# Kernel optimization log

Hardware: AMD Instinct MI355X
Metric: run time of the kernel (lower is better)

## Reference

```python
import jax, jax.numpy as jnp
import numpy as np

B, F, NL = 4096, 1024, 24          # batch, layer width (=in/out features), num hidden layers
TOTAL = F * (NL + 2)               # total DAG nodes: sources + NL hidden ranks + sinks(=last rank)


def setup_inputs() -> dict:
    key = jax.random.key(0)
    k1, k2, k3 = jax.random.split(key, 3)
    x = jax.random.normal(k1, (B, F), jnp.float32)
    # weights incl. bias row; kaiming-ish scale
    W = jax.random.normal(k2, (NL, F + 1, F), jnp.float32) * (1.0 / np.sqrt(F))
    # random 0/1 connectivity mask (requires_grad=False in original); bias row always 1
    M = jax.random.bernoulli(k3, 0.5, (NL, F + 1, F)).astype(jnp.float32)
    M = M.at[:, -1, :].set(1.0)
    sources = jnp.arange(F, dtype=jnp.int32)
    rank = jnp.arange(NL, dtype=jnp.int32)[:, None]
    col = jnp.arange(F, dtype=jnp.int32)[None, :]
    layers_idx = (rank + 1) * F + col   # node ids of rank i+1
    preds_idx = rank * F + col          # predecessors = previous rank
    return {"x": x, "W": W, "M": M, "sources": sources,
            "layers_idx": layers_idx, "preds_idx": preds_idx}


def reference(x, W, M, sources, layers_idx, preds_idx):
    # activations buffer over all DAG nodes
    acts = jnp.zeros((x.shape[0], TOTAL), x.dtype)
    acts = acts.at[:, sources].set(x)
    ones = jnp.ones((x.shape[0], 1), x.dtype)  # bias column

    def step(acts, layer):
        Wi, Mi, li, pi = layer
        h = jnp.concatenate([acts[:, pi], ones], axis=1)   # gather preds + bias
        out = jax.nn.relu(h @ (Mi * Wi))                    # masked GEMM + activation
        acts = acts.at[:, li].set(out)                      # scatter into node activations
        return acts, None

    acts, _ = jax.lax.scan(step, acts, (W, M, layers_idx, preds_idx))
    return acts[:, layers_idx[-1]]  # sinks = last rank
```

## Files before the change

kernel.cpp:

```cpp
#include <hip/hip_runtime.h>
#include <cstdint>
#include <cstddef>

#define NLAYERS 24
#define BATCH   4096
#define FEAT    1024

typedef _Float16 half_t;
typedef half_t half8 __attribute__((ext_vector_type(8)));
typedef float  f32x4 __attribute__((ext_vector_type(4)));

__device__ __forceinline__ void gload_lds16(const void* g, void* l) {
    __builtin_amdgcn_global_load_lds(
        (__attribute__((address_space(1))) void*)(void*)g,
        (__attribute__((address_space(3))) void*)l,
        16, 0, 0);
}

__global__ __launch_bounds__(256) void prep_weights(
    const float* __restrict__ W, const float* __restrict__ M,
    half_t* __restrict__ WmT)
{
    __shared__ float tile[64][65];

    const int bid = blockIdx.x;
    const int l   = bid >> 8;
    const int t   = bid & 255;
    const int k0  = (t >> 4) * 64;
    const int n0  = (t & 15) * 64;
    const size_t lbase = (size_t)l * 1025 * 1024;

    const int tid = threadIdx.x;
    const int rr  = tid >> 4;
    const int c4  = (tid & 15) * 4;

#pragma unroll
    for (int i = 0; i < 4; ++i) {
        const int row = rr + i * 16;
        const size_t g = lbase + (size_t)(k0 + row) * 1024 + (n0 + c4);
        const float4 w4 = *(const float4*)(W + g);
        const float4 m4 = *(const float4*)(M + g);
        tile[row][c4 + 0] = w4.x * m4.x;
        tile[row][c4 + 1] = w4.y * m4.y;
        tile[row][c4 + 2] = w4.z * m4.z;
        tile[row][c4 + 3] = w4.w * m4.w;
    }
    __syncthreads();

    const int n   = tid >> 2;
    const int k16 = (tid & 3) * 16;
    half8 lo, hi;
#pragma unroll
    for (int j = 0; j < 8; ++j) {
        lo[j] = (half_t)tile[k16 + j][n];
        hi[j] = (half_t)tile[k16 + 8 + j][n];
    }
    const size_t o = (size_t)l * 1024 * 1024 + (size_t)(n0 + n) * 1024 + (k0 + k16);
    *(half8*)(WmT + o)     = lo;
    *(half8*)(WmT + o + 8) = hi;
}

__global__ __launch_bounds__(256) void prep_bias(
    const float* __restrict__ W, float* __restrict__ bias)
{
    const int i = blockIdx.x * 256 + threadIdx.x;
    const int l = i >> 10;
    const int n = i & 1023;
    bias[i] = W[(size_t)l * 1025 * 1024 + (size_t)1024 * 1024 + n];
}

__global__ __launch_bounds__(256) void prep_xcast(
    const float* __restrict__ x, half_t* __restrict__ a0)
{
    const size_t i = ((size_t)blockIdx.x * 256 + threadIdx.x) * 8;
    const float4 u = *(const float4*)(x + i);
    const float4 v = *(const float4*)(x + i + 4);
    half8 h;
    h[0] = (half_t)u.x; h[1] = (half_t)u.y; h[2] = (half_t)u.z; h[3] = (half_t)u.w;
    h[4] = (half_t)v.x; h[5] = (half_t)v.y; h[6] = (half_t)v.z; h[7] = (half_t)v.w;
    *(half8*)(a0 + i) = h;
}

template <int LAST>
__global__ __launch_bounds__(256, 2) void gemm_layer(
    const half_t* __restrict__ A,
    const half_t* __restrict__ Bt,
    const float*  __restrict__ bias,
    half_t* __restrict__ Ch,
    float*  __restrict__ Cf)
{
    __shared__ half_t As[128 * 32];
    __shared__ half_t Bs[64 * 32];

    const int tid  = threadIdx.x;
    const int bid  = blockIdx.x;
    const int bm   = bid >> 4;
    const int bn   = bid & 15;
    const int lane = tid & 63;
    const int q    = lane >> 4;
    const int r    = lane & 15;
    const int w    = tid >> 6;
    const int wr   = w >> 1;
    const int wc   = w & 1;

    const half_t* Ab = A  + (size_t)bm * 128 * 1024;
    const half_t* Bb = Bt + (size_t)bn * 64 * 1024;

    const int srow = tid >> 2;
    const int scol = (tid & 3) * 8;
    const int wbase = (tid & 192) * 8;

    const int aoff = (wr * 64 + r) * 32 + q * 8;
    const int boff = (wc * 32 + r) * 32 + q * 8;

    f32x4 acc[4][2];
#pragma unroll
    for (int m = 0; m < 4; ++m)
#pragma unroll
        for (int n = 0; n < 2; ++n)
            acc[m][n] = (f32x4){0.f, 0.f, 0.f, 0.f};

    for (int kt = 0; kt < 32; ++kt) {
        const int k0 = kt * 32;
        __syncthreads();
        gload_lds16(Ab + (size_t)srow * 1024 + k0 + scol,        As + wbase);
        gload_lds16(Ab + (size_t)(64 + srow) * 1024 + k0 + scol, As + 2048 + wbase);
        gload_lds16(Bb + (size_t)srow * 1024 + k0 + scol,        Bs + wbase);
        __syncthreads();

        half8 a[4], b[2];
#pragma unroll
        for (int m = 0; m < 4; ++m) a[m] = *(const half8*)(As + aoff + m * 512);
#pragma unroll
        for (int n = 0; n < 2; ++n) b[n] = *(const half8*)(Bs + boff + n * 512);
#pragma unroll
        for (int m = 0; m < 4; ++m)
#pragma unroll
            for (int n = 0; n < 2; ++n)
                acc[m][n] = __builtin_amdgcn_mfma_f32_16x16x32_f16(a[m], b[n], acc[m][n], 0, 0, 0);
    }

    const int colb = bn * 64 + wc * 32 + r;
    const int rowb = bm * 128 + wr * 64 + q * 4;
#pragma unroll
    for (int n = 0; n < 2; ++n) {
        const int col = colb + n * 16;
        const float bv = bias[col];
#pragma unroll
        for (int m = 0; m < 4; ++m) {
            const int row = rowb + m * 16;
#pragma unroll
            for (int t = 0; t < 4; ++t) {
                float v = acc[m][n][t] + bv;
                v = v > 0.f ? v : 0.f;
                if (LAST) Cf[(size_t)(row + t) * 1024 + col] = v;
                else      Ch[(size_t)(row + t) * 1024 + col] = (half_t)v;
            }
        }
    }
}

extern "C" void kernel_launch(void* const* d_in, const int* in_sizes, int n_in,
                              void* d_out, int out_size, void* d_ws, size_t ws_size,
                              hipStream_t stream)
{
    const float* x = (const float*)d_in[0];
    const float* W = (const float*)d_in[1];
    const float* M = (const float*)d_in[2];
    float* out = (float*)d_out;

    half_t* WmT  = (half_t*)d_ws;
    float*  bias = (float*)(WmT + (size_t)NLAYERS * 1024 * 1024);
    half_t* act0 = (half_t*)(bias + NLAYERS * 1024);
    half_t* act1 = act0 + (size_t)BATCH * FEAT;

    prep_weights<<<dim3(NLAYERS * 256), dim3(256), 0, stream>>>(W, M, WmT);
    prep_bias   <<<dim3(96),            dim3(256), 0, stream>>>(W, bias);
    prep_xcast  <<<dim3(2048),          dim3(256), 0, stream>>>(x, act0);

    half_t* cur = act0;
    half_t* nxt = act1;
    for (int l = 0; l < NLAYERS; ++l) {
        const half_t* Wl = WmT + (size_t)l * 1024 * 1024;
        const float*  bl = bias + l * 1024;
        if (l == NLAYERS - 1) {
            gemm_layer<1><<<dim3(512), dim3(256), 0, stream>>>(cur, Wl, bl, (half_t*)nullptr, out);
        } else {
            gemm_layer<0><<<dim3(512), dim3(256), 0, stream>>>(cur, Wl, bl, nxt, (float*)nullptr);
        }
        half_t* tmp = cur; cur = nxt; nxt = tmp;
    }
}
```

Measured before the change: 736.2 us.

## Enlarge GEMM tile to 128x128 with double-buffered LDS and K=64 steps

The per-layer GEMM block tile grows from 128x64 to 128x128, so each wave computes 4x4 MFMA tiles and both operands get more reuse per byte loaded. LDS is now double-buffered: the next K=64 slab is staged with global_load_lds while the current one is consumed, leaving one barrier per iteration. The shared-memory layout becomes a fragment-ordered swizzle so each lane reads contiguous 16-byte chunks. In exchange, only 256 blocks are launched on a 256-CU part, and more registers and LDS per block lower occupancy.

```diff
diff --git a/kernel.cpp b/kernel.cpp
--- a/kernel.cpp
+++ b/kernel.cpp
@@ -82,20 +82,20 @@
 }
 
 template <int LAST>
-__global__ __launch_bounds__(256, 2) void gemm_layer(
+__global__ __launch_bounds__(256) void gemm_layer(
     const half_t* __restrict__ A,
     const half_t* __restrict__ Bt,
     const float*  __restrict__ bias,
     half_t* __restrict__ Ch,
     float*  __restrict__ Cf)
 {
-    __shared__ half_t As[128 * 32];
-    __shared__ half_t Bs[64 * 32];
+    __shared__ half_t As[2][8192];
+    __shared__ half_t Bs[2][8192];
 
     const int tid  = threadIdx.x;
     const int bid  = blockIdx.x;
-    const int bm   = bid >> 4;
-    const int bn   = bid & 15;
+    const int bm   = bid >> 3;
+    const int bn   = bid & 7;
     const int lane = tid & 63;
     const int q    = lane >> 4;
     const int r    = lane & 15;
@@ -104,46 +104,82 @@
     const int wc   = w & 1;
 
     const half_t* Ab = A  + (size_t)bm * 128 * 1024;
-    const half_t* Bb = Bt + (size_t)bn * 64 * 1024;
-
-    const int srow = tid >> 2;
-    const int scol = (tid & 3) * 8;
-    const int wbase = (tid & 192) * 8;
-
-    const int aoff = (wr * 64 + r) * 32 + q * 8;
-    const int boff = (wc * 32 + r) * 32 + q * 8;
-
-    f32x4 acc[4][2];
+    const half_t* Bb = Bt + (size_t)bn * 128 * 1024;
+
+    const int sc_r  = tid & 15;
+    const int sc_q8 = ((tid >> 4) & 3) * 8;
+
+    f32x4 acc[4][4];
 #pragma unroll
     for (int m = 0; m < 4; ++m)
 #pragma unroll
-        for (int n = 0; n < 2; ++n)
+        for (int n = 0; n < 4; ++n)
             acc[m][n] = (f32x4){0.f, 0.f, 0.f, 0.f};
 
-    for (int kt = 0; kt < 32; ++kt) {
-        const int k0 = kt * 32;
+#define STAGE(ABUF, BBUF, K0)                                                   \
+    {                                                                           \
+        _Pragma("unroll")                                                       \
+        for (int rd = 0; rd < 4; ++rd) {                                        \
+            const int chunk = rd * 256 + tid;                                   \
+            const int kb    = (chunk >> 6) & 1;                                 \
+            const int rb    = chunk >> 7;                                       \
+            const int row   = rb * 16 + sc_r;                                   \
+            const int kc    = (K0) + kb * 32 + sc_q8;                           \
+            const int base  = (rd * 256 + (tid & 192)) * 8;                     \
+            gload_lds16(Ab + (size_t)row * 1024 + kc, (ABUF) + base);           \
+            gload_lds16(Bb + (size_t)row * 1024 + kc, (BBUF) + base);           \
+        }                                                                       \
+    }
+
+    STAGE(As[0], Bs[0], 0)
+
+    const int lane8 = lane * 8;
+    int cur = 0;
+
+    for (int kt = 0; kt < 16; ++kt) {
         __syncthreads();
-        gload_lds16(Ab + (size_t)srow * 1024 + k0 + scol,        As + wbase);
-        gload_lds16(Ab + (size_t)(64 + srow) * 1024 + k0 + scol, As + 2048 + wbase);
-        gload_lds16(Bb + (size_t)srow * 1024 + k0 + scol,        Bs + wbase);
-        __syncthreads();
-
-        half8 a[4], b[2];
-#pragma unroll
-        for (int m = 0; m < 4; ++m) a[m] = *(const half8*)(As + aoff + m * 512);
-#pragma unroll
-        for (int n = 0; n < 2; ++n) b[n] = *(const half8*)(Bs + boff + n * 512);
+        if (kt < 15) {
+            half_t* An = As[cur ^ 1];
+            half_t* Bn = Bs[cur ^ 1];
+            const int k0n = (kt + 1) * 64;
+            STAGE(An, Bn, k0n)
+        }
+
+        const half_t* Ac = As[cur];
+        const half_t* Bc = Bs[cur];
+
+        half8 a0[4], a1[4], b0[4], b1[4];
+#pragma unroll
+        for (int m = 0; m < 4; ++m) {
+            const int sb = (wr * 4 + m) * 2;
+            a0[m] = *(const half8*)(Ac + (sb + 0) * 512 + lane8);
+            a1[m] = *(const half8*)(Ac + (sb + 1) * 512 + lane8);
+        }
+#pragma unroll
+        for (int n = 0; n < 4; ++n) {
+            const int sb = (wc * 4 + n) * 2;
+            b0[n] = *(const half8*)(Bc + (sb + 0) * 512 + lane8);
+            b1[n] = *(const half8*)(Bc + (sb + 1) * 512 + lane8);
+        }
 #pragma unroll
         for (int m = 0; m < 4; ++m)
 #pragma unroll
-            for (int n = 0; n < 2; ++n)
-                acc[m][n] = __builtin_amdgcn_mfma_f32_16x16x32_f16(a[m], b[n], acc[m][n], 0, 0, 0);
-    }
-
-    const int colb = bn * 64 + wc * 32 + r;
+            for (int n = 0; n < 4; ++n)
+                acc[m][n] = __builtin_amdgcn_mfma_f32_16x16x32_f16(a0[m], b0[n], acc[m][n], 0, 0, 0);
+#pragma unroll
+        for (int m = 0; m < 4; ++m)
+#pragma unroll
+            for (int n = 0; n < 4; ++n)
+                acc[m][n] = __builtin_amdgcn_mfma_f32_16x16x32_f16(a1[m], b1[n], acc[m][n], 0, 0, 0);
+
+        cur ^= 1;
+    }
+#undef STAGE
+
+    const int colb = bn * 128 + wc * 64 + r;
     const int rowb = bm * 128 + wr * 64 + q * 4;
 #pragma unroll
-    for (int n = 0; n < 2; ++n) {
+    for (int n = 0; n < 4; ++n) {
         const int col = colb + n * 16;
         const float bv = bias[col];
 #pragma unroll
@@ -184,9 +220,9 @@
         const half_t* Wl = WmT + (size_t)l * 1024 * 1024;
         const float*  bl = bias + l * 1024;
         if (l == NLAYERS - 1) {
-            gemm_layer<1><<<dim3(512), dim3(256), 0, stream>>>(cur, Wl, bl, (half_t*)nullptr, out);
+            gemm_layer<1><<<dim3(256), dim3(256), 0, stream>>>(cur, Wl, bl, (half_t*)nullptr, out);
         } else {
-            gemm_layer<0><<<dim3(512), dim3(256), 0, stream>>>(cur, Wl, bl, nxt, (float*)nullptr);
+            gemm_layer<0><<<dim3(256), dim3(256), 0, stream>>>(cur, Wl, bl, nxt, (float*)nullptr);
         }
         half_t* tmp = cur; cur = nxt; nxt = tmp;
     }
```

Result: slower. 1.010 ms (+37.2%).

## Double-buffer LDS tiles with K=64 stages and fragment-ordered layout

Applied to the files above, without the earlier changes.

The GEMM layer kernel now keeps two LDS buffers, so the global-to-LDS loads for the next K step are issued before the MFMAs on the current buffer. This cuts the two barriers per iteration to one. The K tile grows from 32 to 64, which halves the loop trip count. LDS data is now stored in MFMA-fragment order, so each lane reads a contiguous 16 bytes at lane*8, replacing the strided row reads that likely caused bank conflicts. In exchange the kernel uses three times as much shared memory, about 48KB per block, which may limit how many blocks fit per CU.

```diff
diff --git a/kernel.cpp b/kernel.cpp
--- a/kernel.cpp
+++ b/kernel.cpp
@@ -89,8 +89,8 @@
     half_t* __restrict__ Ch,
     float*  __restrict__ Cf)
 {
-    __shared__ half_t As[128 * 32];
-    __shared__ half_t Bs[64 * 32];
+    __shared__ half_t As[2][8192];
+    __shared__ half_t Bs[2][4096];
 
     const int tid  = threadIdx.x;
     const int bid  = blockIdx.x;
@@ -106,12 +106,9 @@
     const half_t* Ab = A  + (size_t)bm * 128 * 1024;
     const half_t* Bb = Bt + (size_t)bn * 64 * 1024;
 
-    const int srow = tid >> 2;
-    const int scol = (tid & 3) * 8;
-    const int wbase = (tid & 192) * 8;
-
-    const int aoff = (wr * 64 + r) * 32 + q * 8;
-    const int boff = (wc * 32 + r) * 32 + q * 8;
+    const int sc_r  = tid & 15;
+    const int sc_q8 = ((tid >> 4) & 3) * 8;
+    const int wv    = tid >> 6;
 
     f32x4 acc[4][2];
 #pragma unroll
@@ -120,25 +117,66 @@
         for (int n = 0; n < 2; ++n)
             acc[m][n] = (f32x4){0.f, 0.f, 0.f, 0.f};
 
-    for (int kt = 0; kt < 32; ++kt) {
-        const int k0 = kt * 32;
+#define STAGE(ABUF, BBUF, K0)                                                   \
+    {                                                                           \
+        _Pragma("unroll")                                                       \
+        for (int rd = 0; rd < 4; ++rd) {                                        \
+            const int s   = rd * 4 + wv;                     \
+            const int rb  = s >> 1;                                             \
+            const int kb  = s & 1;                                              \
+            const int row = rb * 16 + sc_r;                                     \
+            const int kc  = (K0) + kb * 32 + sc_q8;                             \
+            gload_lds16(Ab + (size_t)row * 1024 + kc,                           \
+                        (ABUF) + (rd * 256 + (tid & 192)) * 8);                 \
+        }                                                                       \
+        _Pragma("unroll")                                                       \
+        for (int rd = 0; rd < 2; ++rd) {                                        \
+            const int s   = rd * 4 + wv;                      \
+            const int rb  = s >> 1;                                             \
+            const int kb  = s & 1;                                              \
+            const int row = rb * 16 + sc_r;                                     \
+            const int kc  = (K0) + kb * 32 + sc_q8;                             \
+            gload_lds16(Bb + (size_t)row * 1024 + kc,                           \
+                        (BBUF) + (rd * 256 + (tid & 192)) * 8);                 \
+        }                                                                       \
+    }
+
+    STAGE(As[0], Bs[0], 0)
+
+    const int lane8 = lane * 8;
+    int cur = 0;
+
+    for (int kt = 0; kt < 16; ++kt) {
         __syncthreads();
-        gload_lds16(Ab + (size_t)srow * 1024 + k0 + scol,        As + wbase);
-        gload_lds16(Ab + (size_t)(64 + srow) * 1024 + k0 + scol, As + 2048 + wbase);
-        gload_lds16(Bb + (size_t)srow * 1024 + k0 + scol,        Bs + wbase);
-        __syncthreads();
-
-        half8 a[4], b[2];
-#pragma unroll
-        for (int m = 0; m < 4; ++m) a[m] = *(const half8*)(As + aoff + m * 512);
-#pragma unroll
-        for (int n = 0; n < 2; ++n) b[n] = *(const half8*)(Bs + boff + n * 512);
-#pragma unroll
-        for (int m = 0; m < 4; ++m)
+        if (kt < 15) {
+            STAGE(As[cur ^ 1], Bs[cur ^ 1], (kt + 1) * 64)
+        }
+
+        const half_t* Ac = As[cur];
+        const half_t* Bc = Bs[cur];
+
+        half8 a[2][4], b[2][2];
+#pragma unroll
+        for (int kb = 0; kb < 2; ++kb) {
+#pragma unroll
+            for (int m = 0; m < 4; ++m)
+                a[kb][m] = *(const half8*)(Ac + ((wr * 4 + m) * 2 + kb) * 512 + lane8);
 #pragma unroll
             for (int n = 0; n < 2; ++n)
-                acc[m][n] = __builtin_amdgcn_mfma_f32_16x16x32_f16(a[m], b[n], acc[m][n], 0, 0, 0);
-    }
+                b[kb][n] = *(const half8*)(Bc + ((wc * 2 + n) * 2 + kb) * 512 + lane8);
+        }
+#pragma unroll
+        for (int kb = 0; kb < 2; ++kb)
+#pragma unroll
+            for (int m = 0; m < 4; ++m)
+#pragma unroll
+                for (int n = 0; n < 2; ++n)
+                    acc[m][n] = __builtin_amdgcn_mfma_f32_16x16x32_f16(
+                        a[kb][m], b[kb][n], acc[m][n], 0, 0, 0);
+
+        cur ^= 1;
+    }
+#undef STAGE
 
     const int colb = bn * 64 + wc * 32 + r;
     const int rowb = bm * 128 + wr * 64 + q * 4;
```

Result: slower. 889.0 us (+20.8%).

## Triple-buffer LDS with async global-to-LDS loads and K=64 tiles in GEMM

Applied to the files above, without the earlier changes.

Replaces the single-buffered K=32 loop, which synchronised twice per step, with a three-stage ring of LDS buffers holding K=64 tiles. Loads for future stages are issued with global_load_lds while MFMAs run on the current stage, using vmcnt waits and a single barrier per stage. Fragment reads use inline ds_read_b128 with immediate offsets in an MFMA-friendly layout. The cost is larger LDS use (72KB per block), which may limit the two-blocks-per-CU occupancy target, plus fragile hand-written waitcnt and scheduling barriers.

```diff
diff --git a/kernel.cpp b/kernel.cpp
--- a/kernel.cpp
+++ b/kernel.cpp
@@ -81,6 +81,9 @@
     *(half8*)(a0 + i) = h;
 }
 
+#define DSR(dst, addr, OFF) \
+    asm volatile("ds_read_b128 %0, %1 offset:" OFF : "=v"(dst) : "v"(addr))
+
 template <int LAST>
 __global__ __launch_bounds__(256, 2) void gemm_layer(
     const half_t* __restrict__ A,
@@ -89,8 +92,8 @@
     half_t* __restrict__ Ch,
     float*  __restrict__ Cf)
 {
-    __shared__ half_t As[128 * 32];
-    __shared__ half_t Bs[64 * 32];
+    __shared__ half_t As0[8192], As1[8192], As2[8192];
+    __shared__ half_t Bs0[4096], Bs1[4096], Bs2[4096];
 
     const int tid  = threadIdx.x;
     const int bid  = blockIdx.x;
@@ -106,12 +109,18 @@
     const half_t* Ab = A  + (size_t)bm * 128 * 1024;
     const half_t* Bb = Bt + (size_t)bn * 64 * 1024;
 
-    const int srow = tid >> 2;
-    const int scol = (tid & 3) * 8;
-    const int wbase = (tid & 192) * 8;
-
-    const int aoff = (wr * 64 + r) * 32 + q * 8;
-    const int boff = (wc * 32 + r) * 32 + q * 8;
+    const int sc_r  = tid & 15;
+    const int sc_q8 = ((tid >> 4) & 3) * 8;
+    const int wv    = tid >> 6;
+
+    const uint32_t As0u = (uint32_t)(uintptr_t)(void*)As0;
+    const uint32_t As1u = (uint32_t)(uintptr_t)(void*)As1;
+    const uint32_t As2u = (uint32_t)(uintptr_t)(void*)As2;
+    const uint32_t Bs0u = (uint32_t)(uintptr_t)(void*)Bs0;
+    const uint32_t Bs1u = (uint32_t)(uintptr_t)(void*)Bs1;
+    const uint32_t Bs2u = (uint32_t)(uintptr_t)(void*)Bs2;
+    const uint32_t aoffw = (uint32_t)(wr * 8192 + lane * 16);
+    const uint32_t boffw = (uint32_t)(wc * 4096 + lane * 16);
 
     f32x4 acc[4][2];
 #pragma unroll
@@ -120,25 +129,83 @@
         for (int n = 0; n < 2; ++n)
             acc[m][n] = (f32x4){0.f, 0.f, 0.f, 0.f};
 
-    for (int kt = 0; kt < 32; ++kt) {
-        const int k0 = kt * 32;
-        __syncthreads();
-        gload_lds16(Ab + (size_t)srow * 1024 + k0 + scol,        As + wbase);
-        gload_lds16(Ab + (size_t)(64 + srow) * 1024 + k0 + scol, As + 2048 + wbase);
-        gload_lds16(Bb + (size_t)srow * 1024 + k0 + scol,        Bs + wbase);
-        __syncthreads();
-
-        half8 a[4], b[2];
-#pragma unroll
-        for (int m = 0; m < 4; ++m) a[m] = *(const half8*)(As + aoff + m * 512);
-#pragma unroll
-        for (int n = 0; n < 2; ++n) b[n] = *(const half8*)(Bs + boff + n * 512);
-#pragma unroll
-        for (int m = 0; m < 4; ++m)
-#pragma unroll
-            for (int n = 0; n < 2; ++n)
-                acc[m][n] = __builtin_amdgcn_mfma_f32_16x16x32_f16(a[m], b[n], acc[m][n], 0, 0, 0);
-    }
+#define STAGE6(K0, SA, SB)                                                     \
+    {                                                                          \
+        _Pragma("unroll")                                                      \
+        for (int rd = 0; rd < 4; ++rd) {                                       \
+            const int s   = rd * 4 + wv;                                       \
+            const int row = (s >> 1) * 16 + sc_r;                              \
+            const int kc  = (K0) + (s & 1) * 32 + sc_q8;                       \
+            gload_lds16(Ab + (size_t)row * 1024 + kc,                          \
+                        (SA) + (rd * 256 + (tid & 192)) * 8);                  \
+        }                                                                      \
+        _Pragma("unroll")                                                      \
+        for (int rd = 0; rd < 2; ++rd) {                                       \
+            const int s   = rd * 4 + wv;                                       \
+            const int row = (s >> 1) * 16 + sc_r;                              \
+            const int kc  = (K0) + (s & 1) * 32 + sc_q8;                       \
+            gload_lds16(Bb + (size_t)row * 1024 + kc,                          \
+                        (SB) + (rd * 256 + (tid & 192)) * 8);                  \
+        }                                                                      \
+    }
+
+#define COMPUTE(RAu, RBu)                                                      \
+    {                                                                          \
+        half8 a[2][4], b[2][2];                                                \
+        const uint32_t aA = (RAu) + aoffw;                                     \
+        const uint32_t aB = (RBu) + boffw;                                     \
+        DSR(a[0][0], aA, "0");    DSR(a[1][0], aA, "1024");                    \
+        DSR(a[0][1], aA, "2048"); DSR(a[1][1], aA, "3072");                    \
+        DSR(a[0][2], aA, "4096"); DSR(a[1][2], aA, "5120");                    \
+        DSR(a[0][3], aA, "6144"); DSR(a[1][3], aA, "7168");                    \
+        DSR(b[0][0], aB, "0");    DSR(b[1][0], aB, "1024");                    \
+        DSR(b[0][1], aB, "2048"); DSR(b[1][1], aB, "3072");                    \
+        asm volatile("s_waitcnt lgkmcnt(0)" ::: "memory");                     \
+        __builtin_amdgcn_sched_barrier(0);                                     \
+        _Pragma("unroll")                                                      \
+        for (int kb = 0; kb < 2; ++kb)                                         \
+            _Pragma("unroll")                                                  \
+            for (int m = 0; m < 4; ++m)                                        \
+                _Pragma("unroll")                                              \
+                for (int n = 0; n < 2; ++n)                                    \
+                    acc[m][n] = __builtin_amdgcn_mfma_f32_16x16x32_f16(        \
+                        a[kb][m], b[kb][n], acc[m][n], 0, 0, 0);               \
+        __builtin_amdgcn_sched_barrier(0);                                     \
+    }
+
+#define SYNC6() { asm volatile("s_waitcnt vmcnt(6)" ::: "memory");             \
+                  __builtin_amdgcn_s_barrier();                                \
+                  __builtin_amdgcn_sched_barrier(0); }
+#define SYNC0() { asm volatile("s_waitcnt vmcnt(0)" ::: "memory");             \
+                  __builtin_amdgcn_s_barrier();                                \
+                  __builtin_amdgcn_sched_barrier(0); }
+
+    STAGE6(0,  As0, Bs0)
+    STAGE6(64, As1, Bs1)
+    SYNC6()
+
+    for (int t = 0; t < 5; ++t) {
+        STAGE6((3 * t + 2) * 64, As2, Bs2)
+        COMPUTE(As0u, Bs0u)
+        SYNC6()
+        STAGE6((3 * t + 3) * 64, As0, Bs0)
+        COMPUTE(As1u, Bs1u)
+        SYNC6()
+        if (t < 4) {
+            STAGE6((3 * t + 4) * 64, As1, Bs1)
+            COMPUTE(As2u, Bs2u)
+            SYNC6()
+        } else {
+            COMPUTE(As2u, Bs2u)
+            SYNC0()
+        }
+    }
+    COMPUTE(As0u, Bs0u)
+
+#undef STAGE6
+#undef COMPUTE
+#undef SYNC6
+#undef SYNC0
 
     const int colb = bn * 64 + wc * 32 + r;
     const int rowb = bm * 128 + wr * 64 + q * 4;
```

After: 840.8 us. 1.14x slower.
